# Optimization experiments

Hardware: AMD Instinct MI355X
Metric: run time of the kernel (lower is better)

## Reference

```python
import jax, jax.numpy as jnp
import numpy as np

B, N, D = 4, 1024, 2048
H_Q, H_KV = 16, 4
D_HEAD = D // H_Q            # 128
GROUPS = H_Q // H_KV         # 4
ROPE_BASE = 10000.0


def rms_norm(x, w, eps):
    # normalize over last dim (d_head), learnable scale w
    ms = jnp.mean(jnp.square(x), axis=-1, keepdims=True)
    return x * jax.lax.rsqrt(ms + eps) * w


def apply_rope(t, pos):
    # t: (B, H, N, d). Half-split RoPE rotation.
    d = t.shape[-1]
    inv_freq = 1.0 / (ROPE_BASE ** (jnp.arange(0, d, 2, dtype=jnp.float32) / d))  # (d/2,)
    ang = pos.astype(jnp.float32)[:, None] * inv_freq[None, :]                     # (N, d/2)
    cos, sin = jnp.cos(ang), jnp.sin(ang)                                          # (N, d/2)
    t1, t2 = t[..., : d // 2], t[..., d // 2 :]
    return jnp.concatenate([t1 * cos - t2 * sin, t2 * cos + t1 * sin], axis=-1)


def setup_inputs() -> dict:
    key = jax.random.key(0)
    ks = jax.random.split(key, 4)
    x = jax.random.normal(ks[0], (B, N, D), dtype=jnp.float32)
    w_qkv = jax.random.normal(ks[1], (D_HEAD * (H_Q + 2 * H_KV), D), dtype=jnp.float32) * (D ** -0.5)
    w_out = jax.random.normal(ks[2], (D, D), dtype=jnp.float32) * (D ** -0.5)
    q_norm_w = jnp.ones((D_HEAD,), dtype=jnp.float32)
    k_norm_w = jnp.ones((D_HEAD,), dtype=jnp.float32)
    mask = jnp.triu(jnp.ones((N, N), dtype=bool), k=1)  # True = masked (causal)
    pos = jnp.arange(N, dtype=jnp.int64) if jax.config.jax_enable_x64 else jnp.arange(N, dtype=jnp.int32)
    return {"x": x, "mask": mask, "pos": pos, "w_qkv": w_qkv, "w_out": w_out,
            "q_norm_w": q_norm_w, "k_norm_w": k_norm_w}


def reference(x, mask, pos, w_qkv, w_out, q_norm_w, k_norm_w):
    eps = jnp.finfo(x.dtype).eps
    scale = D_HEAD ** -0.5
    # fused QKV projection, split into heads
    qkv = jnp.einsum('bnd,ed->bne', x, w_qkv)                       # (B, N, (Hq+2Hkv)*d)
    qkv = qkv.reshape(B, N, H_Q + 2 * H_KV, D_HEAD).transpose(0, 2, 1, 3)
    q, k, v = jnp.split(qkv, [H_Q, H_Q + H_KV], axis=1)             # (B,Hq,N,d),(B,Hkv,N,d)x2
    # qk RMSNorm
    q = rms_norm(q, q_norm_w, eps)
    k = rms_norm(k, k_norm_w, eps)
    # RoPE
    q = apply_rope(q, pos)
    k = apply_rope(k, pos)
    # GQA: repeat kv heads across groups
    k = jnp.repeat(k, GROUPS, axis=1)                               # (B, Hq, N, d)
    v = jnp.repeat(v, GROUPS, axis=1)
    # manual attention (non-flash path)
    scores = jnp.einsum('bhqd,bhkd->bhqk', q, k) * scale            # (B, Hq, N, N)
    scores = jnp.where(mask, -jnp.inf, scores)
    attn = jax.nn.softmax(scores, axis=-1)
    y = jnp.einsum('bhqk,bhkd->bhqd', attn, v)                      # (B, Hq, N, d)
    y = y.transpose(0, 2, 1, 3).reshape(B, N, D)
    return jnp.einsum('bnd,ed->bne', y, w_out)                      # out_proj
```

## Files before the change

### kernel.cpp

```cpp
#include <hip/hip_runtime.h>
#include <cstdint>
#include <cstddef>

#define B_   4
#define N_   1024
#define D_   2048
#define HQ_  16
#define HKV_ 4
#define DH_  128
#define E_   3072

#define SCALE_ 0.08838834764831845

typedef __attribute__((ext_vector_type(8))) short frag16;
typedef __attribute__((ext_vector_type(4))) float fragf4;
#define MFMA16(a, b, c) __builtin_amdgcn_mfma_f32_16x16x32_bf16(a, b, c, 0, 0, 0)

__device__ __forceinline__ short f2bf(float f) {
  union { float f; uint32_t u; } a; a.f = f;
  uint32_t r = (a.u + 0x7fffu + ((a.u >> 16) & 1u)) >> 16;
  return (short)r;
}
__device__ __forceinline__ short f2bf_t(float f) {
  union { float f; uint32_t u; } a; a.f = f;
  return (short)(a.u >> 16);
}
__device__ __forceinline__ float bf2f(unsigned short s) {
  union { uint32_t u; float f; } a;
  a.u = ((uint32_t)s) << 16;
  return a.f;
}
__device__ __forceinline__ void async_copy16(const void* g, void* l) {
  __builtin_amdgcn_global_load_lds(
      (const __attribute__((address_space(1))) void*)g,
      (__attribute__((address_space(3))) void*)l, 16, 0, 0);
}

__global__ __launch_bounds__(256) void f2bf3r(
    const float* __restrict__ s0, short* __restrict__ d0, int b0,
    const float* __restrict__ s1, short* __restrict__ d1, int b1,
    const float* __restrict__ s2, short* __restrict__ d2, int b2,
    const int* __restrict__ pos, float2* __restrict__ tab) {
  int bx = blockIdx.x;
  const int btot = b0 + b1 + b2;
  if (bx < btot) {
    const float* s; short* d;
    if (bx < b0)           { s = s0; d = d0; }
    else if (bx < b0 + b1) { s = s1; d = d1; bx -= b0; }
    else                   { s = s2; d = d2; bx -= b0 + b1; }
    const int i = (bx * 256 + threadIdx.x) * 8;
    float4 a = *(const float4*)(s + i);
    float4 b = *(const float4*)(s + i + 4);
    union { frag16 f; short sh[8]; } u;
    u.sh[0] = f2bf(a.x); u.sh[1] = f2bf(a.y); u.sh[2] = f2bf(a.z); u.sh[3] = f2bf(a.w);
    u.sh[4] = f2bf(b.x); u.sh[5] = f2bf(b.y); u.sh[6] = f2bf(b.z); u.sh[7] = f2bf(b.w);
    *(frag16*)(d + i) = u.f;
  } else {
    const int idx = (bx - btot) * 256 + threadIdx.x;
    const int seq = idx >> 6, dd = idx & 63;
    const float invf = (float)exp2(-(double)dd * 0.20762050593046014);
    const float ang = (float)pos[seq] * invf;
    float2 cs; cs.x = cosf(ang); cs.y = sinf(ang);
    tab[idx] = cs;
  }
}

__global__ __launch_bounds__(256) void gemm_qkv(
    const short* __restrict__ A, const short* __restrict__ Wt,
    short* __restrict__ qkvb, short* __restrict__ vtg,
    const float2* __restrict__ tab,
    const float* __restrict__ qw, const float* __restrict__ kw) {
  __shared__ __align__(16) short smem[17920];
  short* As = smem;
  short* Bs = smem + 8192;

  const int bid = blockIdx.x;
  const int xcd = bid & 7, j = bid >> 3;
  const int m0 = (j & 31) * 128;
  const int n0 = (xcd * 3 + (j >> 5)) * 128;

  const int tid = threadIdx.x;
  const int lane = tid & 63;
  const int w = tid >> 6;
  const int ln = lane & 15, g = lane >> 4;
  const int wm = (w >> 1) * 64, wn = (w & 1) * 64;

  const int srow = lane >> 3;
  const int schunk = ((lane & 7) ^ srow) * 8;
  const int l7 = ln & 7;

  fragf4 acc[4][4];
#pragma unroll
  for (int i = 0; i < 4; ++i)
#pragma unroll
    for (int jj = 0; jj < 4; ++jj) acc[i][jj] = (fragf4){0.f, 0.f, 0.f, 0.f};

  for (int k0 = 0; k0 < D_; k0 += 64) {
    __syncthreads();
#pragma unroll
    for (int i = 0; i < 4; ++i) {
      const int rbase = w * 32 + i * 8;
      const int r = rbase + srow;
      async_copy16(A  + (size_t)(m0 + r) * D_ + k0 + schunk, &As[rbase * 64]);
      async_copy16(Wt + (size_t)(n0 + r) * D_ + k0 + schunk, &Bs[rbase * 64]);
    }
    __syncthreads();

    frag16 af[2][4], bf[2][4];
#pragma unroll
    for (int c = 0; c < 2; ++c) {
      const int pc = (((c << 2) | g) ^ l7) * 8;
#pragma unroll
      for (int t = 0; t < 4; ++t) {
        af[c][t] = *(const frag16*)&As[(wm + t * 16 + ln) * 64 + pc];
        bf[c][t] = *(const frag16*)&Bs[(wn + t * 16 + ln) * 64 + pc];
      }
    }
#pragma unroll
    for (int c = 0; c < 2; ++c)
#pragma unroll
      for (int i = 0; i < 4; ++i)
#pragma unroll
        for (int jj = 0; jj < 4; ++jj)
          acc[i][jj] = MFMA16(af[c][i], bf[c][jj], acc[i][jj]);
  }

  const int hh = n0 >> 7;
  const int b  = m0 >> 10;
  const int seq0 = m0 & 1023;
  short* T = smem;
  float* Sred = (float*)&smem[17408];

  __syncthreads();

  if (hh < 20) {
    float rs[4][4];
#pragma unroll
    for (int i = 0; i < 4; ++i)
#pragma unroll
      for (int r = 0; r < 4; ++r) {
        float t = 0.f;
#pragma unroll
        for (int jj = 0; jj < 4; ++jj) t += acc[i][jj][r] * acc[i][jj][r];
        rs[i][r] = t;
      }
#pragma unroll
    for (int off = 1; off <= 8; off <<= 1)
#pragma unroll
      for (int i = 0; i < 4; ++i)
#pragma unroll
        for (int r = 0; r < 4; ++r) rs[i][r] += __shfl_xor(rs[i][r], off);
    if (ln == 0) {
#pragma unroll
      for (int i = 0; i < 4; ++i)
#pragma unroll
        for (int r = 0; r < 4; ++r)
          Sred[(w & 1) * 128 + wm + i * 16 + 4 * g + r] = rs[i][r];
    }
    __syncthreads();

    const float* wnv = (hh < 16) ? qw : kw;
    float wv[4];
#pragma unroll
    for (int jj = 0; jj < 4; ++jj) wv[jj] = wnv[wn + jj * 16 + ln];
#pragma unroll
    for (int i = 0; i < 4; ++i)
#pragma unroll
      for (int r = 0; r < 4; ++r) {
        const int row = wm + i * 16 + 4 * g + r;
        const float tot = Sred[row] + Sred[128 + row];
        const float rms = rsqrtf(tot * (1.0f / 128.0f) + 1.1920928955078125e-07f);
#pragma unroll
        for (int jj = 0; jj < 4; ++jj)
          T[row * 136 + wn + jj * 16 + ln] = f2bf(acc[i][jj][r] * rms * wv[jj]);
      }
    __syncthreads();

    const int d0 = (tid & 31) * 2, rg = tid >> 5;
#pragma unroll
    for (int rr = 0; rr < 16; ++rr) {
      const int row = rg * 16 + rr;
      ushort2 u1 = *(const ushort2*)&T[row * 136 + d0];
      ushort2 u2 = *(const ushort2*)&T[row * 136 + d0 + 64];
      float4 cs = *(const float4*)&tab[(seq0 + row) * 64 + d0];
      const float v1a = bf2f(u1.x), v1b = bf2f(u1.y);
      const float v2a = bf2f(u2.x), v2b = bf2f(u2.y);
      ushort2 o1, o2;
      o1.x = (unsigned short)f2bf(v1a * cs.x - v2a * cs.y);
      o1.y = (unsigned short)f2bf(v1b * cs.z - v2b * cs.w);
      o2.x = (unsigned short)f2bf(v2a * cs.x + v1a * cs.y);
      o2.y = (unsigned short)f2bf(v2b * cs.z + v1b * cs.w);
      short* dst = qkvb + ((size_t)b * N_ + seq0 + row) * E_ + hh * DH_ + d0;
      *(ushort2*)dst = o1;
      *(ushort2*)(dst + 64) = o2;
    }
  } else {
#pragma unroll
    for (int i = 0; i < 4; ++i)
#pragma unroll
      for (int jj = 0; jj < 4; ++jj)
#pragma unroll
        for (int r = 0; r < 4; ++r)
          T[(wn + jj * 16 + ln) * 136 + wm + i * 16 + 4 * g + r] =
              f2bf(acc[i][jj][r]);
    __syncthreads();

    const int d = tid >> 1, halfi = tid & 1;
    short* dst = vtg + ((size_t)(b * HKV_ + (hh - 20)) * DH_ + d) * N_ +
                 seq0 + halfi * 64;
#pragma unroll
    for (int c = 0; c < 8; ++c)
      *(frag16*)(dst + c * 8) = *(const frag16*)&T[d * 136 + halfi * 64 + c * 8];
  }
}

template <typename OutT>
__global__ __launch_bounds__(256) void gemm_mfma(const short* __restrict__ A,
                                                 const short* __restrict__ Wt,
                                                 OutT* __restrict__ C,
                                                 int Nc, int K, int ncpx) {
  __shared__ __align__(16) short As[128][64];
  __shared__ __align__(16) short Bs[128][64];

  const int bid = blockIdx.x;
  const int xcd = bid & 7, j = bid >> 3;
  const int m0 = (j & 31) * 128;
  const int n0 = (xcd * ncpx + (j >> 5)) * 128;

  const int tid = threadIdx.x;
  const int lane = tid & 63;
  const int w = tid >> 6;
  const int ln = lane & 15, g = lane >> 4;
  const int wm = (w >> 1) * 64, wn = (w & 1) * 64;

  const int srow = lane >> 3;
  const int schunk = ((lane & 7) ^ srow) * 8;
  const int l7 = ln & 7;

  fragf4 acc[4][4];
#pragma unroll
  for (int i = 0; i < 4; ++i)
#pragma unroll
    for (int jj = 0; jj < 4; ++jj) acc[i][jj] = (fragf4){0.f, 0.f, 0.f, 0.f};

  for (int k0 = 0; k0 < K; k0 += 64) {
    __syncthreads();
#pragma unroll
    for (int i = 0; i < 4; ++i) {
      const int rbase = w * 32 + i * 8;
      const int r = rbase + srow;
      async_copy16(A  + (size_t)(m0 + r) * K + k0 + schunk, &As[rbase][0]);
      async_copy16(Wt + (size_t)(n0 + r) * K + k0 + schunk, &Bs[rbase][0]);
    }
    __syncthreads();

    frag16 af[2][4], bf[2][4];
#pragma unroll
    for (int c = 0; c < 2; ++c) {
      const int pc = (((c << 2) | g) ^ l7) * 8;
#pragma unroll
      for (int t = 0; t < 4; ++t) {
        af[c][t] = *(const frag16*)&As[wm + t * 16 + ln][pc];
        bf[c][t] = *(const frag16*)&Bs[wn + t * 16 + ln][pc];
      }
    }
#pragma unroll
    for (int c = 0; c < 2; ++c)
#pragma unroll
      for (int i = 0; i < 4; ++i)
#pragma unroll
        for (int jj = 0; jj < 4; ++jj)
          acc[i][jj] = MFMA16(af[c][i], bf[c][jj], acc[i][jj]);
  }

#pragma unroll
  for (int i = 0; i < 4; ++i) {
#pragma unroll
    for (int jj = 0; jj < 4; ++jj) {
#pragma unroll
      for (int r = 0; r < 4; ++r) {
        const size_t idx = (size_t)(m0 + wm + i * 16 + 4 * g + r) * Nc +
                           (n0 + wn + jj * 16 + ln);
        if constexpr (sizeof(OutT) == 2) C[idx] = f2bf(acc[i][jj][r]);
        else                             C[idx] = acc[i][jj][r];
      }
    }
  }
}

__global__ __launch_bounds__(256) void attn_mfma(const short* __restrict__ qkvb,
                                                 const short* __restrict__ vtg,
                                                 short* __restrict__ yb) {
  const int bx = blockIdx.x;
  const int qt2 = 31 - (bx >> 4);
  const int id = bx & 15;
  const int kh = id & 3, b = id >> 2;
  const int q0 = qt2 * 32;

  __shared__ __align__(16) short lds_[27648];
  const int VT0 = 8192, PS0 = 16384;

  const int tid = threadIdx.x;
  const int lane = tid & 63;
  const int w = tid >> 6;
  const int ln = lane & 15, g = lane >> 4, g8 = g * 8, l7 = ln & 7;
  const int h = kh * 4 + w;
  const int psw = PS0 + w * 2816;

  const short* qb = qkvb + (size_t)b * N_ * E_ + h * DH_;
  const short* kb = qkvb + (size_t)b * N_ * E_ + D_ + kh * DH_;
  const short* vt = vtg + (size_t)(b * HKV_ + kh) * DH_ * N_;

  frag16 qf[2][4];
#pragma unroll
  for (int t = 0; t < 2; ++t) {
    const short* qrow = qb + (size_t)(q0 + 16 * t + ln) * E_ + g8;
#pragma unroll
    for (int c = 0; c < 4; ++c) qf[t][c] = *(const frag16*)(qrow + c * 32);
  }

  frag16 ones;
#pragma unroll
  for (int jx = 0; jx < 8; ++jx) ones[jx] = (short)0x3F80;

  fragf4 o[2][8], ol[2];
#pragma unroll
  for (int t = 0; t < 2; ++t) {
    ol[t] = (fragf4){0.f, 0.f, 0.f, 0.f};
#pragma unroll
    for (int dt = 0; dt < 8; ++dt) o[t][dt] = (fragf4){0.f, 0.f, 0.f, 0.f};
  }

  const float SC2 = (float)(SCALE_ * 1.4426950408889634);
  const float MB2 = (float)(12.0 * 1.4426950408889634);

  const int krow = tid >> 2, kgrp = tid & 3;
  const int vrow = tid >> 1, vgrp = tid & 1;

  const int ntiles = (q0 + 95) >> 6;
  for (int kt = 0; kt < ntiles; ++kt) {
    const int kbase = kt * 64;
    __syncthreads();
    {
      const short* src = kb + (size_t)(kbase + krow) * E_ + kgrp * 32;
      const int r7 = krow & 7;
#pragma unroll
      for (int i = 0; i < 4; ++i) {
        const int lc = kgrp * 4 + i;
        *(frag16*)&lds_[krow * 128 + (lc ^ r7) * 8] = *(const frag16*)(src + i * 8);
      }
    }
    {
      const short* src = vt + (size_t)vrow * N_ + kbase + vgrp * 32;
      const int r7 = vrow & 7;
#pragma unroll
      for (int i = 0; i < 4; ++i) {
        const int lc = vgrp * 4 + i;
        *(frag16*)&lds_[VT0 + vrow * 64 + (lc ^ r7) * 8] = *(const frag16*)(src + i * 8);
      }
    }
    __syncthreads();

    fragf4 s[2][4];
#pragma unroll
    for (int t = 0; t < 2; ++t)
#pragma unroll
      for (int st = 0; st < 4; ++st) s[t][st] = (fragf4){0.f, 0.f, 0.f, 0.f};
#pragma unroll
    for (int c = 0; c < 4; ++c) {
      const int pc = ((c * 4 + g) ^ l7) * 8;
#pragma unroll
      for (int st = 0; st < 4; ++st) {
        frag16 kf = *(const frag16*)&lds_[(st * 16 + ln) * 128 + pc];
        s[0][st] = MFMA16(qf[0][c], kf, s[0][st]);
        s[1][st] = MFMA16(qf[1][c], kf, s[1][st]);
      }
    }

#pragma unroll
    for (int t = 0; t < 2; ++t) {
      const int qbase = q0 + 16 * t;
      const bool full = (kbase + 63) <= qbase;
#pragma unroll
      for (int st = 0; st < 4; ++st) {
        const int kg = kbase + st * 16 + ln;
        const int po = psw + (st >> 1) * 48 + (st & 1) * 16 + ln;
#pragma unroll
        for (int r2 = 0; r2 < 4; ++r2) {
          float sv = s[t][st][r2];
          if (!full && kg > qbase + 4 * g + r2) sv = -1.0e30f;
          const float p = exp2f(fmaf(sv, SC2, -MB2));
          lds_[po + (16 * t + 4 * g + r2) * 88] = f2bf_t(p);
        }
      }
    }

    frag16 pf[2][2];
#pragma unroll
    for (int t = 0; t < 2; ++t)
#pragma unroll
      for (int hh = 0; hh < 2; ++hh)
        pf[t][hh] = *(const frag16*)&lds_[psw + (16 * t + ln) * 88 + hh * 48 + g8];
#pragma unroll
    for (int dt = 0; dt < 8; ++dt) {
#pragma unroll
      for (int hh = 0; hh < 2; ++hh) {
        const int pv = ((hh * 4 + g) ^ l7) * 8;
        frag16 vf = *(const frag16*)&lds_[VT0 + (dt * 16 + ln) * 64 + pv];
        o[0][dt] = MFMA16(pf[0][hh], vf, o[0][dt]);
        o[1][dt] = MFMA16(pf[1][hh], vf, o[1][dt]);
      }
    }
#pragma unroll
    for (int t = 0; t < 2; ++t) {
      ol[t] = MFMA16(pf[t][0], ones, ol[t]);
      ol[t] = MFMA16(pf[t][1], ones, ol[t]);
    }
  }

#pragma unroll
  for (int t = 0; t < 2; ++t) {
#pragma unroll
    for (int r2 = 0; r2 < 4; ++r2) {
      const float inv = 1.0f / ol[t][r2];
      short* yrow = yb + ((size_t)b * N_ + q0 + 16 * t + 4 * g + r2) * D_ + h * DH_;
#pragma unroll
      for (int dt = 0; dt < 8; ++dt) yrow[dt * 16 + ln] = f2bf(o[t][dt][r2] * inv);
    }
  }
}

extern "C" void kernel_launch(void* const* d_in, const int* in_sizes, int n_in,
                              void* d_out, int out_size, void* d_ws, size_t ws_size,
                              hipStream_t stream) {
  const float* x     = (const float*)d_in[0];
  const int*   pos   = (const int*)d_in[2];
  const float* w_qkv = (const float*)d_in[3];
  const float* w_out = (const float*)d_in[4];
  const float* qw    = (const float*)d_in[5];
  const float* kw    = (const float*)d_in[6];
  float* out = (float*)d_out;

  short* qkvb = (short*)d_ws;
  short* yb   = qkvb + (size_t)B_ * N_ * E_;
  short* xb   = yb   + (size_t)B_ * N_ * D_;
  short* wqb  = xb   + (size_t)B_ * N_ * D_;
  short* wob  = wqb  + (size_t)E_ * D_;

  short*  vtg = (short*)d_out;
  float2* tab = (float2*)((short*)d_out + 2097152);

  const int bx_ = (B_ * N_ * D_) / 2048;
  const int bwq = (E_ * D_) / 2048;
  const int bwo = (D_ * D_) / 2048;
  f2bf3r<<<bx_ + bwq + bwo + 256, 256, 0, stream>>>(
      x, xb, bx_, w_qkv, wqb, bwq, w_out, wob, bwo, pos, tab);

  gemm_qkv<<<768, 256, 0, stream>>>(xb, wqb, qkvb, vtg, tab, qw, kw);

  attn_mfma<<<512, 256, 0, stream>>>(qkvb, vtg, yb);

  gemm_mfma<float><<<512, 256, 0, stream>>>(yb, wob, out, D_, D_, 2);
}
```

Baseline: 309.7 us.

## Halve attention query tile per block, pad LDS layouts, vectorize RoPE epilogue

The attention kernel now handles 16 query rows per wave instead of 32 and launches twice as many blocks, which is meant to improve causal load balance and occupancy. K, V and P tiles in LDS switch from XOR swizzling to padded row strides, and the row-sum is taken from a ones row stored in LDS rather than a register fragment. The QKV epilogue uses a 132-element padded stride and processes four elements per thread in the RoPE pass. The trade-off is that each K/V tile is reused by half as many query rows, so global/LDS traffic per unit of work increases.

```diff
diff --git a/kernel.cpp b/kernel.cpp
--- a/kernel.cpp
+++ b/kernel.cpp
@@ -13,6 +13,7 @@
 #define SCALE_ 0.08838834764831845
 
 typedef __attribute__((ext_vector_type(8))) short frag16;
+typedef __attribute__((ext_vector_type(4))) short short4v;
 typedef __attribute__((ext_vector_type(4))) float fragf4;
 #define MFMA16(a, b, c) __builtin_amdgcn_mfma_f32_16x16x32_bf16(a, b, c, 0, 0, 0)
 
@@ -25,9 +26,9 @@
   union { float f; uint32_t u; } a; a.f = f;
   return (short)(a.u >> 16);
 }
-__device__ __forceinline__ float bf2f(unsigned short s) {
+__device__ __forceinline__ float bf2f(short s) {
   union { uint32_t u; float f; } a;
-  a.u = ((uint32_t)s) << 16;
+  a.u = ((uint32_t)(uint16_t)s) << 16;
   return a.f;
 }
 __device__ __forceinline__ void async_copy16(const void* g, void* l) {
@@ -70,7 +71,7 @@
     short* __restrict__ qkvb, short* __restrict__ vtg,
     const float2* __restrict__ tab,
     const float* __restrict__ qw, const float* __restrict__ kw) {
-  __shared__ __align__(16) short smem[17920];
+  __shared__ __align__(16) short smem[17408];
   short* As = smem;
   short* Bs = smem + 8192;
 
@@ -129,7 +130,7 @@
   const int b  = m0 >> 10;
   const int seq0 = m0 & 1023;
   short* T = smem;
-  float* Sred = (float*)&smem[17408];
+  float* Sred = (float*)&smem[16896];
 
   __syncthreads();
 
@@ -172,27 +173,30 @@
         const float rms = rsqrtf(tot * (1.0f / 128.0f) + 1.1920928955078125e-07f);
 #pragma unroll
         for (int jj = 0; jj < 4; ++jj)
-          T[row * 136 + wn + jj * 16 + ln] = f2bf(acc[i][jj][r] * rms * wv[jj]);
-      }
-    __syncthreads();
-
-    const int d0 = (tid & 31) * 2, rg = tid >> 5;
-#pragma unroll
-    for (int rr = 0; rr < 16; ++rr) {
-      const int row = rg * 16 + rr;
-      ushort2 u1 = *(const ushort2*)&T[row * 136 + d0];
-      ushort2 u2 = *(const ushort2*)&T[row * 136 + d0 + 64];
-      float4 cs = *(const float4*)&tab[(seq0 + row) * 64 + d0];
-      const float v1a = bf2f(u1.x), v1b = bf2f(u1.y);
-      const float v2a = bf2f(u2.x), v2b = bf2f(u2.y);
-      ushort2 o1, o2;
-      o1.x = (unsigned short)f2bf(v1a * cs.x - v2a * cs.y);
-      o1.y = (unsigned short)f2bf(v1b * cs.z - v2b * cs.w);
-      o2.x = (unsigned short)f2bf(v2a * cs.x + v1a * cs.y);
-      o2.y = (unsigned short)f2bf(v2b * cs.z + v1b * cs.w);
+          T[row * 132 + wn + jj * 16 + ln] = f2bf(acc[i][jj][r] * rms * wv[jj]);
+      }
+    __syncthreads();
+
+    const int d0 = (tid & 15) * 4, rt = tid >> 4;
+#pragma unroll
+    for (int rr = 0; rr < 8; ++rr) {
+      const int row = rt * 8 + rr;
+      short4v lo = *(const short4v*)&T[row * 132 + d0];
+      short4v hi = *(const short4v*)&T[row * 132 + d0 + 64];
+      float4 cs01 = *(const float4*)&tab[(seq0 + row) * 64 + d0];
+      float4 cs23 = *(const float4*)&tab[(seq0 + row) * 64 + d0 + 2];
+      float c[4] = {cs01.x, cs01.z, cs23.x, cs23.z};
+      float s[4] = {cs01.y, cs01.w, cs23.y, cs23.w};
+      short4v olo, ohi;
+#pragma unroll
+      for (int q = 0; q < 4; ++q) {
+        const float a = bf2f(lo[q]), bb = bf2f(hi[q]);
+        olo[q] = f2bf(a * c[q] - bb * s[q]);
+        ohi[q] = f2bf(bb * c[q] + a * s[q]);
+      }
       short* dst = qkvb + ((size_t)b * N_ + seq0 + row) * E_ + hh * DH_ + d0;
-      *(ushort2*)dst = o1;
-      *(ushort2*)(dst + 64) = o2;
+      *(short4v*)dst = olo;
+      *(short4v*)(dst + 64) = ohi;
     }
   } else {
 #pragma unroll
@@ -201,7 +205,7 @@
       for (int jj = 0; jj < 4; ++jj)
 #pragma unroll
         for (int r = 0; r < 4; ++r)
-          T[(wn + jj * 16 + ln) * 136 + wm + i * 16 + 4 * g + r] =
+          T[(wn + jj * 16 + ln) * 132 + wm + i * 16 + 4 * g + r] =
               f2bf(acc[i][jj][r]);
     __syncthreads();
 
@@ -210,7 +214,7 @@
                  seq0 + halfi * 64;
 #pragma unroll
     for (int c = 0; c < 8; ++c)
-      *(frag16*)(dst + c * 8) = *(const frag16*)&T[d * 136 + halfi * 64 + c * 8];
+      *(frag16*)(dst + c * 8) = *(const frag16*)&T[d * 132 + halfi * 64 + c * 8];
   }
 }
 
@@ -292,141 +296,110 @@
                                                  const short* __restrict__ vtg,
                                                  short* __restrict__ yb) {
   const int bx = blockIdx.x;
-  const int qt2 = 31 - (bx >> 4);
+  const int qt = 63 - (bx >> 4);
   const int id = bx & 15;
   const int kh = id & 3, b = id >> 2;
-  const int q0 = qt2 * 32;
-
-  __shared__ __align__(16) short lds_[27648];
-  const int VT0 = 8192, PS0 = 16384;
+  const int q0 = qt * 16;
+
+  __shared__ __align__(16) short lds_[22600];
+  const int VT0 = 8704, PS0 = 17992;
 
   const int tid = threadIdx.x;
   const int lane = tid & 63;
   const int w = tid >> 6;
-  const int ln = lane & 15, g = lane >> 4, g8 = g * 8, l7 = ln & 7;
+  const int ln = lane & 15, g = lane >> 4, g8 = g * 8;
   const int h = kh * 4 + w;
-  const int psw = PS0 + w * 2816;
 
   const short* qb = qkvb + (size_t)b * N_ * E_ + h * DH_;
   const short* kb = qkvb + (size_t)b * N_ * E_ + D_ + kh * DH_;
   const short* vt = vtg + (size_t)(b * HKV_ + kh) * DH_ * N_;
 
-  frag16 qf[2][4];
-#pragma unroll
-  for (int t = 0; t < 2; ++t) {
-    const short* qrow = qb + (size_t)(q0 + 16 * t + ln) * E_ + g8;
-#pragma unroll
-    for (int c = 0; c < 4; ++c) qf[t][c] = *(const frag16*)(qrow + c * 32);
-  }
-
-  frag16 ones;
-#pragma unroll
-  for (int jx = 0; jx < 8; ++jx) ones[jx] = (short)0x3F80;
-
-  fragf4 o[2][8], ol[2];
-#pragma unroll
-  for (int t = 0; t < 2; ++t) {
-    ol[t] = (fragf4){0.f, 0.f, 0.f, 0.f};
-#pragma unroll
-    for (int dt = 0; dt < 8; ++dt) o[t][dt] = (fragf4){0.f, 0.f, 0.f, 0.f};
-  }
+  if (tid < 64) lds_[VT0 + 128 * 72 + tid] = (short)0x3F80;
+
+  frag16 qf[4];
+  {
+    const short* qrow = qb + (size_t)(q0 + ln) * E_ + g8;
+#pragma unroll
+    for (int c = 0; c < 4; ++c) qf[c] = *(const frag16*)(qrow + c * 32);
+  }
+
+  fragf4 o[8], ol = (fragf4){0.f, 0.f, 0.f, 0.f};
+#pragma unroll
+  for (int dt = 0; dt < 8; ++dt) o[dt] = (fragf4){0.f, 0.f, 0.f, 0.f};
 
   const float SC2 = (float)(SCALE_ * 1.4426950408889634);
   const float MB2 = (float)(12.0 * 1.4426950408889634);
 
-  const int krow = tid >> 2, kgrp = tid & 3;
-  const int vrow = tid >> 1, vgrp = tid & 1;
-
-  const int ntiles = (q0 + 95) >> 6;
+  const int ntiles = qt / 4 + 1;
   for (int kt = 0; kt < ntiles; ++kt) {
     const int kbase = kt * 64;
     __syncthreads();
     {
-      const short* src = kb + (size_t)(kbase + krow) * E_ + kgrp * 32;
-      const int r7 = krow & 7;
-#pragma unroll
-      for (int i = 0; i < 4; ++i) {
-        const int lc = kgrp * 4 + i;
-        *(frag16*)&lds_[krow * 128 + (lc ^ r7) * 8] = *(const frag16*)(src + i * 8);
-      }
+      const int r = tid & 63, c = (tid >> 6) * 32;
+      const short* src = kb + (size_t)(kbase + r) * E_ + c;
+#pragma unroll
+      for (int i = 0; i < 4; ++i)
+        *(frag16*)&lds_[r * 136 + c + 8 * i] = *(const frag16*)(src + 8 * i);
     }
     {
-      const short* src = vt + (size_t)vrow * N_ + kbase + vgrp * 32;
-      const int r7 = vrow & 7;
-#pragma unroll
-      for (int i = 0; i < 4; ++i) {
-        const int lc = vgrp * 4 + i;
-        *(frag16*)&lds_[VT0 + vrow * 64 + (lc ^ r7) * 8] = *(const frag16*)(src + i * 8);
-      }
-    }
-    __syncthreads();
-
-    fragf4 s[2][4];
-#pragma unroll
-    for (int t = 0; t < 2; ++t)
-#pragma unroll
-      for (int st = 0; st < 4; ++st) s[t][st] = (fragf4){0.f, 0.f, 0.f, 0.f};
+      const int d = tid & 127, e = tid >> 7;
+      const short* src = vt + (size_t)d * N_ + kbase + e * 32;
+#pragma unroll
+      for (int i = 0; i < 4; ++i)
+        *(frag16*)&lds_[VT0 + d * 72 + e * 32 + 8 * i] = *(const frag16*)(src + 8 * i);
+    }
+    __syncthreads();
+
+    fragf4 s[4];
+#pragma unroll
+    for (int st = 0; st < 4; ++st) s[st] = (fragf4){0.f, 0.f, 0.f, 0.f};
 #pragma unroll
     for (int c = 0; c < 4; ++c) {
-      const int pc = ((c * 4 + g) ^ l7) * 8;
+      frag16 qc = qf[c];
 #pragma unroll
       for (int st = 0; st < 4; ++st) {
-        frag16 kf = *(const frag16*)&lds_[(st * 16 + ln) * 128 + pc];
-        s[0][st] = MFMA16(qf[0][c], kf, s[0][st]);
-        s[1][st] = MFMA16(qf[1][c], kf, s[1][st]);
-      }
-    }
-
-#pragma unroll
-    for (int t = 0; t < 2; ++t) {
-      const int qbase = q0 + 16 * t;
-      const bool full = (kbase + 63) <= qbase;
-#pragma unroll
-      for (int st = 0; st < 4; ++st) {
-        const int kg = kbase + st * 16 + ln;
-        const int po = psw + (st >> 1) * 48 + (st & 1) * 16 + ln;
-#pragma unroll
-        for (int r2 = 0; r2 < 4; ++r2) {
-          float sv = s[t][st][r2];
-          if (!full && kg > qbase + 4 * g + r2) sv = -1.0e30f;
-          const float p = exp2f(fmaf(sv, SC2, -MB2));
-          lds_[po + (16 * t + 4 * g + r2) * 88] = f2bf_t(p);
-        }
-      }
-    }
-
-    frag16 pf[2][2];
-#pragma unroll
-    for (int t = 0; t < 2; ++t)
-#pragma unroll
-      for (int hh = 0; hh < 2; ++hh)
-        pf[t][hh] = *(const frag16*)&lds_[psw + (16 * t + ln) * 88 + hh * 48 + g8];
+        frag16 kf = *(const frag16*)&lds_[(st * 16 + ln) * 136 + c * 32 + g8];
+        s[st] = MFMA16(qc, kf, s[st]);
+      }
+    }
+
+    const bool full = (kbase + 63) <= q0;
+#pragma unroll
+    for (int st = 0; st < 4; ++st) {
+      const int kg = kbase + st * 16 + ln;
+#pragma unroll
+      for (int r2 = 0; r2 < 4; ++r2) {
+        float sv = s[st][r2];
+        if (!full && kg > q0 + 4 * g + r2) sv = -1.0e30f;
+        const float p = exp2f(fmaf(sv, SC2, -MB2));
+        lds_[PS0 + (w * 16 + 4 * g + r2) * 72 + st * 16 + ln] = f2bf_t(p);
+      }
+    }
+
+    frag16 pf0 = *(const frag16*)&lds_[PS0 + (w * 16 + ln) * 72 + g8];
+    frag16 pf1 = *(const frag16*)&lds_[PS0 + (w * 16 + ln) * 72 + 32 + g8];
 #pragma unroll
     for (int dt = 0; dt < 8; ++dt) {
-#pragma unroll
-      for (int hh = 0; hh < 2; ++hh) {
-        const int pv = ((hh * 4 + g) ^ l7) * 8;
-        frag16 vf = *(const frag16*)&lds_[VT0 + (dt * 16 + ln) * 64 + pv];
-        o[0][dt] = MFMA16(pf[0][hh], vf, o[0][dt]);
-        o[1][dt] = MFMA16(pf[1][hh], vf, o[1][dt]);
-      }
-    }
-#pragma unroll
-    for (int t = 0; t < 2; ++t) {
-      ol[t] = MFMA16(pf[t][0], ones, ol[t]);
-      ol[t] = MFMA16(pf[t][1], ones, ol[t]);
-    }
-  }
-
-#pragma unroll
-  for (int t = 0; t < 2; ++t) {
-#pragma unroll
-    for (int r2 = 0; r2 < 4; ++r2) {
-      const float inv = 1.0f / ol[t][r2];
-      short* yrow = yb + ((size_t)b * N_ + q0 + 16 * t + 4 * g + r2) * D_ + h * DH_;
-#pragma unroll
-      for (int dt = 0; dt < 8; ++dt) yrow[dt * 16 + ln] = f2bf(o[t][dt][r2] * inv);
-    }
+      frag16 v0 = *(const frag16*)&lds_[VT0 + (dt * 16 + ln) * 72 + g8];
+      frag16 v1 = *(const frag16*)&lds_[VT0 + (dt * 16 + ln) * 72 + 32 + g8];
+      o[dt] = MFMA16(pf0, v0, o[dt]);
+      o[dt] = MFMA16(pf1, v1, o[dt]);
+    }
+    {
+      frag16 vl0 = *(const frag16*)&lds_[VT0 + (128 + ln) * 72 + g8];
+      frag16 vl1 = *(const frag16*)&lds_[VT0 + (128 + ln) * 72 + 32 + g8];
+      ol = MFMA16(pf0, vl0, ol);
+      ol = MFMA16(pf1, vl1, ol);
+    }
+  }
+
+#pragma unroll
+  for (int r2 = 0; r2 < 4; ++r2) {
+    const float lv = __shfl(ol[r2], lane & 48);
+    const float inv = 1.0f / lv;
+    short* yrow = yb + ((size_t)b * N_ + q0 + 4 * g + r2) * D_ + h * DH_;
+#pragma unroll
+    for (int dt = 0; dt < 8; ++dt) yrow[dt * 16 + ln] = f2bf(o[dt][r2] * inv);
   }
 }
 
@@ -458,7 +431,7 @@
 
   gemm_qkv<<<768, 256, 0, stream>>>(xb, wqb, qkvb, vtg, tab, qw, kw);
 
-  attn_mfma<<<512, 256, 0, stream>>>(qkvb, vtg, yb);
+  attn_mfma<<<1024, 256, 0, stream>>>(qkvb, vtg, yb);
 
   gemm_mfma<float><<<512, 256, 0, stream>>>(yb, wob, out, D_, D_, 2);
 }
```

Result: no change. 304.5 us (-1.7%).
